# Optimization experiments

Hardware: AMD Instinct MI355X
Metric: run time of the kernel (lower is better)

Reference implementation:

```python
import jax, jax.numpy as jnp
import numpy as np

N_GROUPS = 20000
K = 12
C_IN = 256
C_CH = 128
EPS = 1e-5


def _layernorm(x, g, b):
    mu = jnp.mean(x, axis=-1, keepdims=True)
    var = jnp.mean((x - mu) ** 2, axis=-1, keepdims=True)
    return (x - mu) * jax.lax.rsqrt(var + EPS) * g + b


def _linear(x, W, b):
    # torch nn.Linear: y = x @ W.T + b, W: [out, in]
    return x @ W.T + b


def setup_inputs() -> dict:
    key = jax.random.key(0)
    ks = jax.random.split(key, 16)
    nnz = N_GROUPS * K
    s_in = 1.0 / np.sqrt(C_IN)
    s_ch = 1.0 / np.sqrt(C_CH)
    return {
        "values": jax.random.normal(ks[0], (nnz, C_IN), jnp.float32),
        "ln_in_g": jnp.ones((C_IN,), jnp.float32),
        "ln_in_b": jnp.zeros((C_IN,), jnp.float32),
        "W_ga": jax.random.normal(ks[1], (C_CH, C_IN), jnp.float32) * s_in,
        "b_ga": jax.random.normal(ks[2], (C_CH,), jnp.float32) * 0.02,
        "W_la": jax.random.normal(ks[3], (C_CH, C_IN), jnp.float32) * s_in,
        "b_la": jnp.zeros((C_CH,), jnp.float32),
        "W_gb": jax.random.normal(ks[4], (C_CH, C_IN), jnp.float32) * s_in,
        "b_gb": jax.random.normal(ks[5], (C_CH,), jnp.float32) * 0.02,
        "W_lb": jax.random.normal(ks[6], (C_CH, C_IN), jnp.float32) * s_in,
        "b_lb": jnp.zeros((C_CH,), jnp.float32),
        "ln_o_g": jnp.ones((C_CH,), jnp.float32),
        "ln_o_b": jnp.zeros((C_CH,), jnp.float32),
        "W_go": jax.random.normal(ks[7], (C_IN, C_IN), jnp.float32) * s_in,
        "b_go": jax.random.normal(ks[8], (C_IN,), jnp.float32) * 0.02,
        "W_lo": jax.random.normal(ks[9], (C_IN, C_CH), jnp.float32) * s_ch,
        "b_lo": jax.random.normal(ks[10], (C_IN,), jnp.float32) * 0.02,
        "indices": jax.random.randint(ks[11], (4, nnz), 0, 20000, jnp.int64 if jax.config.jax_enable_x64 else jnp.int32),
    }


def reference(values, ln_in_g, ln_in_b, W_ga, b_ga, W_la, b_la, W_gb, b_gb,
              W_lb, b_lb, ln_o_g, ln_o_b, W_go, b_go, W_lo, b_lo, indices):
    nnz = values.shape[0]
    # input layer norm over channel dim of sparse values
    x = _layernorm(values, ln_in_g, ln_in_b)  # [nnz, C_IN]
    # gated projections to channel_dim
    a = jax.nn.sigmoid(_linear(x, W_ga, b_ga)) * _linear(x, W_la, b_la)  # [nnz, C_CH]
    b = jax.nn.sigmoid(_linear(x, W_gb, b_gb)) * _linear(x, W_lb, b_lb)
    a = a.reshape(nnz // K, K, C_CH)
    b = b.reshape(nnz // K, K, C_CH)
    # axis == 1: einsum('iko,jko->iko', a, b) = a * sum_j b[j]
    tri = a * jnp.sum(b, axis=0, keepdims=True)  # [nnz//K, K, C_CH]
    tri = tri.reshape(nnz, C_CH)
    # output: gate on x times linear of normed triangular update
    out = jax.nn.sigmoid(_linear(x, W_go, b_go)) * _linear(
        _layernorm(tri, ln_o_g, ln_o_b), W_lo, b_lo)  # [nnz, C_IN]
    return out
```

## Files before the change

kernel.cpp:

```cpp
#include <hip/hip_runtime.h>


#define NNZ   240000
#define ROWS  64
#define NBLK  (NNZ / ROWS)
#define PSLOTS 32

typedef __attribute__((ext_vector_type(8))) short bf16x8;
typedef __attribute__((ext_vector_type(4))) float f32x4;
typedef __attribute__((ext_vector_type(8))) _Float16 f16x8;

__device__ __forceinline__ unsigned short f2bf(float f) {
  unsigned int u = __float_as_uint(f);
  u += 0x7fffu + ((u >> 16) & 1u);
  return (unsigned short)(u >> 16);
}
__device__ __forceinline__ float bf2f(unsigned short h) {
  return __uint_as_float(((unsigned int)h) << 16);
}

__global__ __launch_bounds__(256) void prep_kernel(
    const float* __restrict__ Wga, const float* __restrict__ Wla,
    const float* __restrict__ Wgb, const float* __restrict__ Wlb,
    const float* __restrict__ Wgo, const float* __restrict__ Wlo,
    unsigned short* __restrict__ wcat, unsigned short* __restrict__ wgo16,
    unsigned short* __restrict__ wlo16, float* __restrict__ bsum,
    float* __restrict__ bpart)
{
  const int tid = blockIdx.x * 256 + threadIdx.x;
  if (tid < 12 * 128) bsum[tid] = 0.f;
  if (tid < PSLOTS * 1536) bpart[tid] = 0.f;
  if (tid < 131072) {
    const int w8 = tid & 7, c = tid >> 3;
    const int m = c & 15, q = (c >> 4) & 3, t = (c >> 6) & 3;
    const int kb = (c >> 8) & 7, wv = c >> 11;
    const int k = kb * 32 + q * 8 + w8;
    const int ch = ((wv & 3) << 5) + ((t & 1) << 4) + m;
    const float* src = (wv < 4) ? (t < 2 ? Wga : Wla) : (t < 2 ? Wgb : Wlb);
    wcat[tid] = f2bf(src[ch * 256 + k]);
  } else if (tid < 196608) {
    const int o = tid - 131072;
    const int w8 = o & 7, c = o >> 3;
    const int m = c & 15, q = (c >> 4) & 3, nt = (c >> 6) & 1;
    const int kb = (c >> 7) & 7, wv = c >> 10;
    wgo16[o] = f2bf(Wgo[(wv * 32 + nt * 16 + m) * 256 + kb * 32 + q * 8 + w8]);
  } else if (tid < 229376) {
    const int o = tid - 196608;
    const int w8 = o & 7, c = o >> 3;
    const int m = c & 15, q = (c >> 4) & 3, nt = (c >> 6) & 1;
    const int kb = (c >> 7) & 3, wv = c >> 9;
    wlo16[o] = f2bf(Wlo[(wv * 32 + nt * 16 + m) * 128 + kb * 32 + q * 8 + w8]);
  }
}

__global__ __launch_bounds__(512, 4) void k1_kernel(
    const float* __restrict__ values,
    const float* __restrict__ ln_g, const float* __restrict__ ln_b,
    const float* __restrict__ b_ga, const float* __restrict__ b_la,
    const float* __restrict__ b_gb, const float* __restrict__ b_lb,
    const float* __restrict__ b_go,
    const unsigned short* __restrict__ wcat,
    const unsigned short* __restrict__ wgo,
    _Float16* __restrict__ g_ws,
    unsigned short* __restrict__ a_ws,
    float* __restrict__ bpart)
{
  __shared__ unsigned short x_lds[ROWS][256];
  __shared__ float b_raw[ROWS][132];
  const int tid = threadIdx.x;
  const int rbase = blockIdx.x * ROWS;

  {
    const int r = tid >> 3, j = tid & 7;
    const size_t grow = (size_t)(rbase + r) * 256;
    float4 v[8];
    float s1 = 0.f, s2 = 0.f;
#pragma unroll
    for (int i = 0; i < 4; i++) {
      const int e = (j + 8 * i) * 8;
      const float4 t0 = *(const float4*)(values + grow + e);
      const float4 t1 = *(const float4*)(values + grow + e + 4);
      v[2 * i] = t0; v[2 * i + 1] = t1;
      s1 += t0.x + t0.y + t0.z + t0.w + t1.x + t1.y + t1.z + t1.w;
      s2 += t0.x * t0.x + t0.y * t0.y + t0.z * t0.z + t0.w * t0.w
          + t1.x * t1.x + t1.y * t1.y + t1.z * t1.z + t1.w * t1.w;
    }
    s1 += __shfl_xor(s1, 1); s1 += __shfl_xor(s1, 2); s1 += __shfl_xor(s1, 4);
    s2 += __shfl_xor(s2, 1); s2 += __shfl_xor(s2, 2); s2 += __shfl_xor(s2, 4);
    const float mu = s1 * (1.f / 256.f);
    const float rstd = rsqrtf(s2 * (1.f / 256.f) - mu * mu + 1e-5f);
    const int jp = j ^ (r & 7);
#pragma unroll
    for (int i = 0; i < 4; i++) {
      const int e = (j + 8 * i) * 8;
      const float4 a0 = v[2 * i], a1 = v[2 * i + 1];
      const float4 g0 = *(const float4*)(ln_g + e);
      const float4 g1 = *(const float4*)(ln_g + e + 4);
      const float4 c0 = *(const float4*)(ln_b + e);
      const float4 c1 = *(const float4*)(ln_b + e + 4);
      bf16x8 h;
      h[0] = (short)f2bf((a0.x - mu) * rstd * g0.x + c0.x);
      h[1] = (short)f2bf((a0.y - mu) * rstd * g0.y + c0.y);
      h[2] = (short)f2bf((a0.z - mu) * rstd * g0.z + c0.z);
      h[3] = (short)f2bf((a0.w - mu) * rstd * g0.w + c0.w);
      h[4] = (short)f2bf((a1.x - mu) * rstd * g1.x + c1.x);
      h[5] = (short)f2bf((a1.y - mu) * rstd * g1.y + c1.y);
      h[6] = (short)f2bf((a1.z - mu) * rstd * g1.z + c1.z);
      h[7] = (short)f2bf((a1.w - mu) * rstd * g1.w + c1.w);
      *(bf16x8*)&x_lds[r][(jp + 8 * i) * 8] = h;
    }
  }
  __syncthreads();

  const int wv = tid >> 6;
  const int lane = tid & 63;
  const int m = lane & 15, q = lane >> 4;

  {
    f32x4 acc[4][4];
#pragma unroll
    for (int a = 0; a < 4; a++)
#pragma unroll
      for (int b = 0; b < 4; b++) acc[a][b] = (f32x4){0.f, 0.f, 0.f, 0.f};

#pragma unroll
    for (int kb = 0; kb < 8; kb++) {
      bf16x8 A[4], B[4];
#pragma unroll
      for (int mt = 0; mt < 4; mt++)
        A[mt] = *(const bf16x8*)&x_lds[mt * 16 + m][((kb * 4 + q) ^ (m & 7)) << 3];
#pragma unroll
      for (int t = 0; t < 4; t++)
        B[t] = *(const bf16x8*)(wcat + ((((wv * 8 + kb) * 4 + t) * 64 + lane) << 3));
#pragma unroll
      for (int t = 0; t < 4; t++)
#pragma unroll
        for (int mt = 0; mt < 4; mt++)
          acc[mt][t] = __builtin_amdgcn_mfma_f32_16x16x32_bf16(A[mt], B[t], acc[mt][t], 0, 0, 0);
    }

    const bool isA = (wv < 4);
    const int chbase = (wv & 3) * 32;
    const float* bgp = isA ? b_ga : b_gb;
    const float* blp = isA ? b_la : b_lb;
#pragma unroll
    for (int t = 0; t < 2; t++) {
      const int ch = chbase + t * 16 + m;
      const float bgv = bgp[ch], blv = blp[ch];
#pragma unroll
      for (int mt = 0; mt < 4; mt++) {
#pragma unroll
        for (int rg = 0; rg < 4; rg++) {
          const int lrow = mt * 16 + q * 4 + rg;
          const float gv = acc[mt][t][rg] + bgv;
          const float lv = acc[mt][t + 2][rg] + blv;
          const float val = lv / (1.f + __expf(-gv));
          if (isA) {
            a_ws[(size_t)(rbase + lrow) * 128 + ch] = f2bf(val);
          } else {
            b_raw[lrow][ch] = val;
          }
        }
      }
    }
  }

  {
    f32x4 g2[4][2];
#pragma unroll
    for (int a = 0; a < 4; a++)
#pragma unroll
      for (int b = 0; b < 2; b++) g2[a][b] = (f32x4){0.f, 0.f, 0.f, 0.f};

#pragma unroll
    for (int kb = 0; kb < 8; kb++) {
      bf16x8 A[4], B[2];
#pragma unroll
      for (int mt = 0; mt < 4; mt++)
        A[mt] = *(const bf16x8*)&x_lds[mt * 16 + m][((kb * 4 + q) ^ (m & 7)) << 3];
#pragma unroll
      for (int nt = 0; nt < 2; nt++)
        B[nt] = *(const bf16x8*)(wgo + ((((wv * 8 + kb) * 2 + nt) * 64 + lane) << 3));
#pragma unroll
      for (int nt = 0; nt < 2; nt++)
#pragma unroll
        for (int mt = 0; mt < 4; mt++)
          g2[mt][nt] = __builtin_amdgcn_mfma_f32_16x16x32_bf16(A[mt], B[nt], g2[mt][nt], 0, 0, 0);
    }

    const int n0 = wv * 32;
    f16x8 hv[4];
#pragma unroll
    for (int nt = 0; nt < 2; nt++) {
      const float bg = b_go[n0 + nt * 16 + m];
#pragma unroll
      for (int mt = 0; mt < 4; mt++) {
#pragma unroll
        for (int rg = 0; rg < 4; rg++) {
          const float gv = g2[mt][nt][rg] + bg;
          const float s = 1.f / (1.f + __expf(-gv));
          const int idx = (mt * 4 + rg) * 2 + nt;
          hv[idx >> 3][idx & 7] = (_Float16)s;
        }
      }
    }
    _Float16* gd = g_ws + ((((size_t)blockIdx.x) * 8 + wv) * 64 + lane) * 32;
#pragma unroll
    for (int i = 0; i < 4; i++)
      *(f16x8*)(gd + i * 8) = hv[i];
  }
  __syncthreads();

  const int rb12 = rbase % 12;
  float* dst = bpart + (blockIdx.x & (PSLOTS - 1)) * 1536;
#pragma unroll
  for (int it = 0; it < 3; it++) {
    const int s = tid + it * 512;
    const int k12 = s >> 7, ch = s & 127;
    int r0 = k12 - rb12; if (r0 < 0) r0 += 12;
    float sum = 0.f;
    for (int r = r0; r < ROWS; r += 12) sum += b_raw[r][ch];
    atomicAdd(&dst[s], sum);
  }
}

__global__ __launch_bounds__(256) void reduce_kernel(
    const float* __restrict__ bpart, float* __restrict__ bsum)
{
  const int c = blockIdx.x * 256 + threadIdx.x;
  float s = 0.f;
#pragma unroll
  for (int sl = 0; sl < PSLOTS; sl++) s += bpart[sl * 1536 + c];
  bsum[c] = s;
}

__global__ __launch_bounds__(512, 6) void k2_kernel(
    const _Float16* __restrict__ g_ws,
    const unsigned short* __restrict__ a_ws,
    const float* __restrict__ bsum,
    const float* __restrict__ ln_g, const float* __restrict__ ln_b,
    const unsigned short* __restrict__ wlo,
    const float* __restrict__ b_lo,
    float* __restrict__ out)
{
  __shared__ unsigned short t_lds[ROWS][128];
  const int tid = threadIdx.x;
  const int rbase = blockIdx.x * ROWS;

  {
    const int r = tid >> 3, j = tid & 7;
    const int row = rbase + r;
    const int k12 = row % 12;
    const unsigned short* ar = a_ws + (size_t)row * 128;
    const float* bs = bsum + k12 * 128;
    float tv[16];
    float s1 = 0.f, s2 = 0.f;
#pragma unroll
    for (int i = 0; i < 2; i++) {
      const int e = (j + 8 * i) * 8;
      const ushort4 a0 = *(const ushort4*)(ar + e);
      const ushort4 a1 = *(const ushort4*)(ar + e + 4);
      const float4 b0 = *(const float4*)(bs + e);
      const float4 b1 = *(const float4*)(bs + e + 4);
      const float t0 = bf2f(a0.x) * b0.x, t1 = bf2f(a0.y) * b0.y;
      const float t2 = bf2f(a0.z) * b0.z, t3 = bf2f(a0.w) * b0.w;
      const float t4 = bf2f(a1.x) * b1.x, t5 = bf2f(a1.y) * b1.y;
      const float t6 = bf2f(a1.z) * b1.z, t7 = bf2f(a1.w) * b1.w;
      tv[8*i+0] = t0; tv[8*i+1] = t1; tv[8*i+2] = t2; tv[8*i+3] = t3;
      tv[8*i+4] = t4; tv[8*i+5] = t5; tv[8*i+6] = t6; tv[8*i+7] = t7;
      s1 += t0 + t1 + t2 + t3 + t4 + t5 + t6 + t7;
      s2 += t0*t0 + t1*t1 + t2*t2 + t3*t3 + t4*t4 + t5*t5 + t6*t6 + t7*t7;
    }
    s1 += __shfl_xor(s1, 1); s1 += __shfl_xor(s1, 2); s1 += __shfl_xor(s1, 4);
    s2 += __shfl_xor(s2, 1); s2 += __shfl_xor(s2, 2); s2 += __shfl_xor(s2, 4);
    const float mu = s1 * (1.f / 128.f);
    const float rstd = rsqrtf(s2 * (1.f / 128.f) - mu * mu + 1e-5f);
    const int jp = j ^ (r & 7);
#pragma unroll
    for (int i = 0; i < 2; i++) {
      const int e = (j + 8 * i) * 8;
      const float4 g0 = *(const float4*)(ln_g + e);
      const float4 g1 = *(const float4*)(ln_g + e + 4);
      const float4 c0 = *(const float4*)(ln_b + e);
      const float4 c1 = *(const float4*)(ln_b + e + 4);
      bf16x8 h;
      h[0] = (short)f2bf((tv[8*i+0] - mu) * rstd * g0.x + c0.x);
      h[1] = (short)f2bf((tv[8*i+1] - mu) * rstd * g0.y + c0.y);
      h[2] = (short)f2bf((tv[8*i+2] - mu) * rstd * g0.z + c0.z);
      h[3] = (short)f2bf((tv[8*i+3] - mu) * rstd * g0.w + c0.w);
      h[4] = (short)f2bf((tv[8*i+4] - mu) * rstd * g1.x + c1.x);
      h[5] = (short)f2bf((tv[8*i+5] - mu) * rstd * g1.y + c1.y);
      h[6] = (short)f2bf((tv[8*i+6] - mu) * rstd * g1.z + c1.z);
      h[7] = (short)f2bf((tv[8*i+7] - mu) * rstd * g1.w + c1.w);
      *(bf16x8*)&t_lds[r][(jp + 8 * i) * 8] = h;
    }
  }
  __syncthreads();

  const int wv = tid >> 6, lane = tid & 63;
  const int m = lane & 15, q = lane >> 4;

  const _Float16* gs = g_ws + ((((size_t)blockIdx.x) * 8 + wv) * 64 + lane) * 32;
  f16x8 gh[4];
#pragma unroll
  for (int i = 0; i < 4; i++)
    gh[i] = *(const f16x8*)(gs + i * 8);

  f32x4 al[4][2];
#pragma unroll
  for (int a = 0; a < 4; a++)
#pragma unroll
    for (int b = 0; b < 2; b++) al[a][b] = (f32x4){0.f, 0.f, 0.f, 0.f};

#pragma unroll
  for (int kb = 0; kb < 4; kb++) {
    bf16x8 A[4], B[2];
#pragma unroll
    for (int mt = 0; mt < 4; mt++)
      A[mt] = *(const bf16x8*)&t_lds[mt * 16 + m][((kb * 4 + q) ^ (m & 7)) << 3];
#pragma unroll
    for (int nt = 0; nt < 2; nt++)
      B[nt] = *(const bf16x8*)(wlo + ((((wv * 4 + kb) * 2 + nt) * 64 + lane) << 3));
#pragma unroll
    for (int nt = 0; nt < 2; nt++)
#pragma unroll
      for (int mt = 0; mt < 4; mt++)
        al[mt][nt] = __builtin_amdgcn_mfma_f32_16x16x32_bf16(A[mt], B[nt], al[mt][nt], 0, 0, 0);
  }

#pragma unroll
  for (int nt = 0; nt < 2; nt++) {
    const int n = wv * 32 + nt * 16 + m;
    const float blo = b_lo[n];
#pragma unroll
    for (int mt = 0; mt < 4; mt++) {
#pragma unroll
      for (int rg = 0; rg < 4; rg++) {
        const int row = rbase + mt * 16 + q * 4 + rg;
        const int idx = (mt * 4 + rg) * 2 + nt;
        const float gval = (float)gh[idx >> 3][idx & 7];
        out[(size_t)row * 256 + n] = gval * (al[mt][nt][rg] + blo);
      }
    }
  }
}

extern "C" void kernel_launch(void* const* d_in, const int* in_sizes, int n_in,
                              void* d_out, int out_size, void* d_ws, size_t ws_size,
                              hipStream_t stream) {
  (void)in_sizes; (void)n_in; (void)out_size; (void)ws_size;
  const float* values  = (const float*)d_in[0];
  const float* ln_in_g = (const float*)d_in[1];
  const float* ln_in_b = (const float*)d_in[2];
  const float* W_ga = (const float*)d_in[3];
  const float* b_ga = (const float*)d_in[4];
  const float* W_la = (const float*)d_in[5];
  const float* b_la = (const float*)d_in[6];
  const float* W_gb = (const float*)d_in[7];
  const float* b_gb = (const float*)d_in[8];
  const float* W_lb = (const float*)d_in[9];
  const float* b_lb = (const float*)d_in[10];
  const float* ln_o_g = (const float*)d_in[11];
  const float* ln_o_b = (const float*)d_in[12];
  const float* W_go = (const float*)d_in[13];
  const float* b_go = (const float*)d_in[14];
  const float* W_lo = (const float*)d_in[15];
  const float* b_lo = (const float*)d_in[16];

  char* ws = (char*)d_ws;
  _Float16*       g_ws  = (_Float16*)      (ws + 0);
  unsigned short* a_ws  = (unsigned short*)(ws + 122880000);
  unsigned short* wcat  = (unsigned short*)(ws + 184320000);
  unsigned short* wgo16 = (unsigned short*)(ws + 184582144);
  unsigned short* wlo16 = (unsigned short*)(ws + 184713216);
  float*          bsum  = (float*)        (ws + 184778752);
  float*          bpart = (float*)        (ws + 184784896);

  hipLaunchKernelGGL(prep_kernel, dim3(896), dim3(256), 0, stream,
                     W_ga, W_la, W_gb, W_lb, W_go, W_lo, wcat, wgo16, wlo16,
                     bsum, bpart);
  hipLaunchKernelGGL(k1_kernel, dim3(NBLK), dim3(512), 0, stream,
                     values, ln_in_g, ln_in_b, b_ga, b_la, b_gb, b_lb, b_go,
                     wcat, wgo16, g_ws, a_ws, bpart);
  hipLaunchKernelGGL(reduce_kernel, dim3(6), dim3(256), 0, stream,
                     bpart, bsum);
  hipLaunchKernelGGL(k2_kernel, dim3(NBLK), dim3(512), 0, stream,
                     g_ws, a_ws, bsum, ln_o_g, ln_o_b, wlo16, b_lo,
                     (float*)d_out);
}
```

Measured before the change: 662.3 us.

## Store x in MFMA fragment layout and drop LDS staging in k2

In k1, x is now written to LDS in MFMA-fragment order, so each lane's A operand becomes one contiguous 16-byte read with no XOR swizzle. The gate workspace changes to a lane-interleaved layout for coalesced stores. k2 is restructured into a 2x4 wave tiling that loads a_ws fragments directly from global memory, computes the layernorm with cross-quad shuffles, and feeds the MFMAs from registers, removing its LDS buffer and a __syncthreads. The cost is higher register pressure, so k2's occupancy hint drops from 6 to 4 blocks, and the fragment-order LDS writes may cause bank conflicts.

```diff
diff --git a/kernel.cpp b/kernel.cpp
--- a/kernel.cpp
+++ b/kernel.cpp
@@ -65,7 +65,7 @@
     unsigned short* __restrict__ a_ws,
     float* __restrict__ bpart)
 {
-  __shared__ unsigned short x_lds[ROWS][256];
+  __shared__ unsigned short x_lds[16384];
   __shared__ float b_raw[ROWS][132];
   const int tid = threadIdx.x;
   const int rbase = blockIdx.x * ROWS;
@@ -89,10 +89,11 @@
     s2 += __shfl_xor(s2, 1); s2 += __shfl_xor(s2, 2); s2 += __shfl_xor(s2, 4);
     const float mu = s1 * (1.f / 256.f);
     const float rstd = rsqrtf(s2 * (1.f / 256.f) - mu * mu + 1e-5f);
-    const int jp = j ^ (r & 7);
+    const int m = r & 15, mt = r >> 4;
 #pragma unroll
     for (int i = 0; i < 4; i++) {
-      const int e = (j + 8 * i) * 8;
+      const int c8 = j + 8 * i;
+      const int e = c8 * 8;
       const float4 a0 = v[2 * i], a1 = v[2 * i + 1];
       const float4 g0 = *(const float4*)(ln_g + e);
       const float4 g1 = *(const float4*)(ln_g + e + 4);
@@ -107,7 +108,8 @@
       h[5] = (short)f2bf((a1.y - mu) * rstd * g1.y + c1.y);
       h[6] = (short)f2bf((a1.z - mu) * rstd * g1.z + c1.z);
       h[7] = (short)f2bf((a1.w - mu) * rstd * g1.w + c1.w);
-      *(bf16x8*)&x_lds[r][(jp + 8 * i) * 8] = h;
+      const int off = (((c8 >> 2) * 4 + mt) * 64 + (c8 & 3) * 16 + m) * 8;
+      *(bf16x8*)&x_lds[off] = h;
     }
   }
   __syncthreads();
@@ -128,7 +130,7 @@
       bf16x8 A[4], B[4];
 #pragma unroll
       for (int mt = 0; mt < 4; mt++)
-        A[mt] = *(const bf16x8*)&x_lds[mt * 16 + m][((kb * 4 + q) ^ (m & 7)) << 3];
+        A[mt] = *(const bf16x8*)&x_lds[((kb * 4 + mt) * 64 + lane) * 8];
 #pragma unroll
       for (int t = 0; t < 4; t++)
         B[t] = *(const bf16x8*)(wcat + ((((wv * 8 + kb) * 4 + t) * 64 + lane) << 3));
@@ -177,7 +179,7 @@
       bf16x8 A[4], B[2];
 #pragma unroll
       for (int mt = 0; mt < 4; mt++)
-        A[mt] = *(const bf16x8*)&x_lds[mt * 16 + m][((kb * 4 + q) ^ (m & 7)) << 3];
+        A[mt] = *(const bf16x8*)&x_lds[((kb * 4 + mt) * 64 + lane) * 8];
 #pragma unroll
       for (int nt = 0; nt < 2; nt++)
         B[nt] = *(const bf16x8*)(wgo + ((((wv * 8 + kb) * 2 + nt) * 64 + lane) << 3));
@@ -204,10 +206,10 @@
         }
       }
     }
-    _Float16* gd = g_ws + ((((size_t)blockIdx.x) * 8 + wv) * 64 + lane) * 32;
+    _Float16* gd = g_ws + ((size_t)blockIdx.x * 8 + wv) * 2048;
 #pragma unroll
     for (int i = 0; i < 4; i++)
-      *(f16x8*)(gd + i * 8) = hv[i];
+      *(f16x8*)(gd + i * 512 + lane * 8) = hv[i];
   }
   __syncthreads();
 
@@ -234,7 +236,7 @@
   bsum[c] = s;
 }
 
-__global__ __launch_bounds__(512, 6) void k2_kernel(
+__global__ __launch_bounds__(512, 4) void k2_kernel(
     const _Float16* __restrict__ g_ws,
     const unsigned short* __restrict__ a_ws,
     const float* __restrict__ bsum,
@@ -243,102 +245,110 @@
     const float* __restrict__ b_lo,
     float* __restrict__ out)
 {
-  __shared__ unsigned short t_lds[ROWS][128];
   const int tid = threadIdx.x;
   const int rbase = blockIdx.x * ROWS;
-
-  {
-    const int r = tid >> 3, j = tid & 7;
-    const int row = rbase + r;
-    const int k12 = row % 12;
-    const unsigned short* ar = a_ws + (size_t)row * 128;
-    const float* bs = bsum + k12 * 128;
-    float tv[16];
+  const int wv = tid >> 6, lane = tid & 63;
+  const int m = lane & 15, q = lane >> 4;
+  const int wr = wv >> 2, wc = wv & 3;
+
+  f16x8 gh[2][2];
+#pragma unroll
+  for (int s = 0; s < 2; s++)
+#pragma unroll
+    for (int c = 0; c < 2; c++)
+      gh[s][c] = *(const f16x8*)(g_ws +
+          (((size_t)blockIdx.x * 8 + wc * 2 + s) * 4 + wr * 2 + c) * 512 + lane * 8);
+
+  bf16x8 afr[2][4];
+#pragma unroll
+  for (int mt = 0; mt < 2; mt++) {
+    const unsigned short* ap =
+        a_ws + (size_t)(rbase + wr * 32 + mt * 16 + m) * 128 + q * 8;
+#pragma unroll
+    for (int kb = 0; kb < 4; kb++)
+      afr[mt][kb] = *(const bf16x8*)(ap + kb * 32);
+  }
+
+  bf16x8 tfr[2][4];
+#pragma unroll
+  for (int mt = 0; mt < 2; mt++) {
+    const int row = rbase + wr * 32 + mt * 16 + m;
+    const float* bs = bsum + (row % 12) * 128 + q * 8;
+    float tv[32];
     float s1 = 0.f, s2 = 0.f;
 #pragma unroll
-    for (int i = 0; i < 2; i++) {
-      const int e = (j + 8 * i) * 8;
-      const ushort4 a0 = *(const ushort4*)(ar + e);
-      const ushort4 a1 = *(const ushort4*)(ar + e + 4);
-      const float4 b0 = *(const float4*)(bs + e);
-      const float4 b1 = *(const float4*)(bs + e + 4);
-      const float t0 = bf2f(a0.x) * b0.x, t1 = bf2f(a0.y) * b0.y;
-      const float t2 = bf2f(a0.z) * b0.z, t3 = bf2f(a0.w) * b0.w;
-      const float t4 = bf2f(a1.x) * b1.x, t5 = bf2f(a1.y) * b1.y;
-      const float t6 = bf2f(a1.z) * b1.z, t7 = bf2f(a1.w) * b1.w;
-      tv[8*i+0] = t0; tv[8*i+1] = t1; tv[8*i+2] = t2; tv[8*i+3] = t3;
-      tv[8*i+4] = t4; tv[8*i+5] = t5; tv[8*i+6] = t6; tv[8*i+7] = t7;
+    for (int kb = 0; kb < 4; kb++) {
+      const float4 b0 = *(const float4*)(bs + kb * 32);
+      const float4 b1 = *(const float4*)(bs + kb * 32 + 4);
+      const bf16x8 a8 = afr[mt][kb];
+      const float t0 = bf2f((unsigned short)a8[0]) * b0.x;
+      const float t1 = bf2f((unsigned short)a8[1]) * b0.y;
+      const float t2 = bf2f((unsigned short)a8[2]) * b0.z;
+      const float t3 = bf2f((unsigned short)a8[3]) * b0.w;
+      const float t4 = bf2f((unsigned short)a8[4]) * b1.x;
+      const float t5 = bf2f((unsigned short)a8[5]) * b1.y;
+      const float t6 = bf2f((unsigned short)a8[6]) * b1.z;
+      const float t7 = bf2f((unsigned short)a8[7]) * b1.w;
+      tv[kb*8+0] = t0; tv[kb*8+1] = t1; tv[kb*8+2] = t2; tv[kb*8+3] = t3;
+      tv[kb*8+4] = t4; tv[kb*8+5] = t5; tv[kb*8+6] = t6; tv[kb*8+7] = t7;
       s1 += t0 + t1 + t2 + t3 + t4 + t5 + t6 + t7;
       s2 += t0*t0 + t1*t1 + t2*t2 + t3*t3 + t4*t4 + t5*t5 + t6*t6 + t7*t7;
     }
-    s1 += __shfl_xor(s1, 1); s1 += __shfl_xor(s1, 2); s1 += __shfl_xor(s1, 4);
-    s2 += __shfl_xor(s2, 1); s2 += __shfl_xor(s2, 2); s2 += __shfl_xor(s2, 4);
+    s1 += __shfl_xor(s1, 16); s1 += __shfl_xor(s1, 32);
+    s2 += __shfl_xor(s2, 16); s2 += __shfl_xor(s2, 32);
     const float mu = s1 * (1.f / 128.f);
     const float rstd = rsqrtf(s2 * (1.f / 128.f) - mu * mu + 1e-5f);
-    const int jp = j ^ (r & 7);
-#pragma unroll
-    for (int i = 0; i < 2; i++) {
-      const int e = (j + 8 * i) * 8;
+#pragma unroll
+    for (int kb = 0; kb < 4; kb++) {
+      const int e = kb * 32 + q * 8;
       const float4 g0 = *(const float4*)(ln_g + e);
       const float4 g1 = *(const float4*)(ln_g + e + 4);
       const float4 c0 = *(const float4*)(ln_b + e);
       const float4 c1 = *(const float4*)(ln_b + e + 4);
       bf16x8 h;
-      h[0] = (short)f2bf((tv[8*i+0] - mu) * rstd * g0.x + c0.x);
-      h[1] = (short)f2bf((tv[8*i+1] - mu) * rstd * g0.y + c0.y);
-      h[2] = (short)f2bf((tv[8*i+2] - mu) * rstd * g0.z + c0.z);
-      h[3] = (short)f2bf((tv[8*i+3] - mu) * rstd * g0.w + c0.w);
-      h[4] = (short)f2bf((tv[8*i+4] - mu) * rstd * g1.x + c1.x);
-      h[5] = (short)f2bf((tv[8*i+5] - mu) * rstd * g1.y + c1.y);
-      h[6] = (short)f2bf((tv[8*i+6] - mu) * rstd * g1.z + c1.z);
-      h[7] = (short)f2bf((tv[8*i+7] - mu) * rstd * g1.w + c1.w);
-      *(bf16x8*)&t_lds[r][(jp + 8 * i) * 8] = h;
-    }
-  }
-  __syncthreads();
-
-  const int wv = tid >> 6, lane = tid & 63;
-  const int m = lane & 15, q = lane >> 4;
-
-  const _Float16* gs = g_ws + ((((size_t)blockIdx.x) * 8 + wv) * 64 + lane) * 32;
-  f16x8 gh[4];
-#pragma unroll
-  for (int i = 0; i < 4; i++)
-    gh[i] = *(const f16x8*)(gs + i * 8);
-
-  f32x4 al[4][2];
-#pragma unroll
-  for (int a = 0; a < 4; a++)
-#pragma unroll
-    for (int b = 0; b < 2; b++) al[a][b] = (f32x4){0.f, 0.f, 0.f, 0.f};
+      h[0] = (short)f2bf((tv[kb*8+0] - mu) * rstd * g0.x + c0.x);
+      h[1] = (short)f2bf((tv[kb*8+1] - mu) * rstd * g0.y + c0.y);
+      h[2] = (short)f2bf((tv[kb*8+2] - mu) * rstd * g0.z + c0.z);
+      h[3] = (short)f2bf((tv[kb*8+3] - mu) * rstd * g0.w + c0.w);
+      h[4] = (short)f2bf((tv[kb*8+4] - mu) * rstd * g1.x + c1.x);
+      h[5] = (short)f2bf((tv[kb*8+5] - mu) * rstd * g1.y + c1.y);
+      h[6] = (short)f2bf((tv[kb*8+6] - mu) * rstd * g1.z + c1.z);
+      h[7] = (short)f2bf((tv[kb*8+7] - mu) * rstd * g1.w + c1.w);
+      tfr[mt][kb] = h;
+    }
+  }
+
+  f32x4 al[2][4];
+#pragma unroll
+  for (int a = 0; a < 2; a++)
+#pragma unroll
+    for (int b = 0; b < 4; b++) al[a][b] = (f32x4){0.f, 0.f, 0.f, 0.f};
 
 #pragma unroll
   for (int kb = 0; kb < 4; kb++) {
-    bf16x8 A[4], B[2];
-#pragma unroll
-    for (int mt = 0; mt < 4; mt++)
-      A[mt] = *(const bf16x8*)&t_lds[mt * 16 + m][((kb * 4 + q) ^ (m & 7)) << 3];
-#pragma unroll
-    for (int nt = 0; nt < 2; nt++)
-      B[nt] = *(const bf16x8*)(wlo + ((((wv * 4 + kb) * 2 + nt) * 64 + lane) << 3));
-#pragma unroll
-    for (int nt = 0; nt < 2; nt++)
-#pragma unroll
-      for (int mt = 0; mt < 4; mt++)
-        al[mt][nt] = __builtin_amdgcn_mfma_f32_16x16x32_bf16(A[mt], B[nt], al[mt][nt], 0, 0, 0);
-  }
-
-#pragma unroll
-  for (int nt = 0; nt < 2; nt++) {
-    const int n = wv * 32 + nt * 16 + m;
+    bf16x8 B[4];
+#pragma unroll
+    for (int nt = 0; nt < 4; nt++)
+      B[nt] = *(const bf16x8*)(wlo +
+          (((((wc * 2 + (nt >> 1)) * 4 + kb) * 2 + (nt & 1)) * 64 + lane) << 3));
+#pragma unroll
+    for (int nt = 0; nt < 4; nt++)
+#pragma unroll
+      for (int mt = 0; mt < 2; mt++)
+        al[mt][nt] = __builtin_amdgcn_mfma_f32_16x16x32_bf16(tfr[mt][kb], B[nt], al[mt][nt], 0, 0, 0);
+  }
+
+#pragma unroll
+  for (int nt = 0; nt < 4; nt++) {
+    const int n = wc * 64 + nt * 16 + m;
     const float blo = b_lo[n];
 #pragma unroll
-    for (int mt = 0; mt < 4; mt++) {
+    for (int mt = 0; mt < 2; mt++) {
 #pragma unroll
       for (int rg = 0; rg < 4; rg++) {
-        const int row = rbase + mt * 16 + q * 4 + rg;
-        const int idx = (mt * 4 + rg) * 2 + nt;
-        const float gval = (float)gh[idx >> 3][idx & 7];
+        const int row = rbase + wr * 32 + mt * 16 + q * 4 + rg;
+        const int il = ((mt * 4 + rg) * 2 + (nt & 1));
+        const float gval = (float)gh[nt >> 1][il >> 3][il & 7];
         out[(size_t)row * 256 + n] = gval * (al[mt][nt][rg] + blo);
       }
     }
```

Result: slower. 1.049 ms (+58.4%).

## Alias k1 LDS buffers, reorder gate GEMM first, coalesce g_ws layout

Applied to the files above, without the earlier changes.

In k1 the output-gate GEMM now runs before the main gated-projection GEMM, which lets x_lds and b_raw share one LDS allocation: the x tile is dead by the time b_raw is written, with a barrier placed between them. The launch-bounds minimum-blocks hint rises from 4 to 8 to raise occupancy. The g_ws gate layout becomes lane-interleaved so its stores and loads coalesce across the wavefront, and k2 loads the a row as one 16-byte vector instead of two 8-byte ones. The higher occupancy target may force register spills, since the 4x4 accumulator tile stays live.

```diff
diff --git a/kernel.cpp b/kernel.cpp
--- a/kernel.cpp
+++ b/kernel.cpp
@@ -53,7 +53,7 @@
   }
 }
 
-__global__ __launch_bounds__(512, 4) void k1_kernel(
+__global__ __launch_bounds__(512, 8) void k1_kernel(
     const float* __restrict__ values,
     const float* __restrict__ ln_g, const float* __restrict__ ln_b,
     const float* __restrict__ b_ga, const float* __restrict__ b_la,
@@ -65,8 +65,9 @@
     unsigned short* __restrict__ a_ws,
     float* __restrict__ bpart)
 {
-  __shared__ unsigned short x_lds[ROWS][256];
-  __shared__ float b_raw[ROWS][132];
+  __shared__ float smem[ROWS * 132];
+  float (*b_raw)[132] = (float(*)[132])smem;
+  unsigned short (*x_lds)[256] = (unsigned short(*)[256])smem;
   const int tid = threadIdx.x;
   const int rbase = blockIdx.x * ROWS;
 
@@ -107,7 +108,8 @@
       h[5] = (short)f2bf((a1.y - mu) * rstd * g1.y + c1.y);
       h[6] = (short)f2bf((a1.z - mu) * rstd * g1.z + c1.z);
       h[7] = (short)f2bf((a1.w - mu) * rstd * g1.w + c1.w);
-      *(bf16x8*)&x_lds[r][(jp + 8 * i) * 8] = h;
+      const int p = (jp + 8 * i) * 8;
+      *(bf16x8*)&x_lds[r][p] = h;
     }
   }
   __syncthreads();
@@ -117,28 +119,75 @@
   const int m = lane & 15, q = lane >> 4;
 
   {
-    f32x4 acc[4][4];
+    f32x4 g2[4][2];
 #pragma unroll
     for (int a = 0; a < 4; a++)
 #pragma unroll
-      for (int b = 0; b < 4; b++) acc[a][b] = (f32x4){0.f, 0.f, 0.f, 0.f};
+      for (int b = 0; b < 2; b++) g2[a][b] = (f32x4){0.f, 0.f, 0.f, 0.f};
 
 #pragma unroll
     for (int kb = 0; kb < 8; kb++) {
-      bf16x8 A[4], B[4];
+      bf16x8 A[4], B[2];
 #pragma unroll
       for (int mt = 0; mt < 4; mt++)
         A[mt] = *(const bf16x8*)&x_lds[mt * 16 + m][((kb * 4 + q) ^ (m & 7)) << 3];
 #pragma unroll
-      for (int t = 0; t < 4; t++)
-        B[t] = *(const bf16x8*)(wcat + ((((wv * 8 + kb) * 4 + t) * 64 + lane) << 3));
-#pragma unroll
-      for (int t = 0; t < 4; t++)
+      for (int nt = 0; nt < 2; nt++)
+        B[nt] = *(const bf16x8*)(wgo + ((((wv * 8 + kb) * 2 + nt) * 64 + lane) << 3));
+#pragma unroll
+      for (int nt = 0; nt < 2; nt++)
 #pragma unroll
         for (int mt = 0; mt < 4; mt++)
-          acc[mt][t] = __builtin_amdgcn_mfma_f32_16x16x32_bf16(A[mt], B[t], acc[mt][t], 0, 0, 0);
-    }
-
+          g2[mt][nt] = __builtin_amdgcn_mfma_f32_16x16x32_bf16(A[mt], B[nt], g2[mt][nt], 0, 0, 0);
+    }
+
+    const int n0 = wv * 32;
+    f16x8 hv[4];
+#pragma unroll
+    for (int nt = 0; nt < 2; nt++) {
+      const float bg = b_go[n0 + nt * 16 + m];
+#pragma unroll
+      for (int mt = 0; mt < 4; mt++) {
+#pragma unroll
+        for (int rg = 0; rg < 4; rg++) {
+          const float gv = g2[mt][nt][rg] + bg;
+          const float s = 1.f / (1.f + __expf(-gv));
+          const int idx = (mt * 4 + rg) * 2 + nt;
+          hv[idx >> 3][idx & 7] = (_Float16)s;
+        }
+      }
+    }
+    _Float16* gd = g_ws + ((size_t)blockIdx.x * 8 + wv) * 2048;
+#pragma unroll
+    for (int i = 0; i < 4; i++)
+      *(f16x8*)(gd + i * 512 + lane * 8) = hv[i];
+  }
+
+  f32x4 acc[4][4];
+#pragma unroll
+  for (int a = 0; a < 4; a++)
+#pragma unroll
+    for (int b = 0; b < 4; b++) acc[a][b] = (f32x4){0.f, 0.f, 0.f, 0.f};
+
+#pragma unroll
+  for (int kb = 0; kb < 8; kb++) {
+    bf16x8 A[4], B[4];
+#pragma unroll
+    for (int mt = 0; mt < 4; mt++)
+      A[mt] = *(const bf16x8*)&x_lds[mt * 16 + m][((kb * 4 + q) ^ (m & 7)) << 3];
+#pragma unroll
+    for (int t = 0; t < 4; t++)
+      B[t] = *(const bf16x8*)(wcat + ((((wv * 8 + kb) * 4 + t) * 64 + lane) << 3));
+#pragma unroll
+    for (int t = 0; t < 4; t++)
+#pragma unroll
+      for (int mt = 0; mt < 4; mt++)
+        acc[mt][t] = __builtin_amdgcn_mfma_f32_16x16x32_bf16(A[mt], B[t], acc[mt][t], 0, 0, 0);
+  }
+
+  __syncthreads();
+
+  {
     const bool isA = (wv < 4);
     const int chbase = (wv & 3) * 32;
     const float* bgp = isA ? b_ga : b_gb;
@@ -164,51 +213,6 @@
       }
     }
   }
-
-  {
-    f32x4 g2[4][2];
-#pragma unroll
-    for (int a = 0; a < 4; a++)
-#pragma unroll
-      for (int b = 0; b < 2; b++) g2[a][b] = (f32x4){0.f, 0.f, 0.f, 0.f};
-
-#pragma unroll
-    for (int kb = 0; kb < 8; kb++) {
-      bf16x8 A[4], B[2];
-#pragma unroll
-      for (int mt = 0; mt < 4; mt++)
-        A[mt] = *(const bf16x8*)&x_lds[mt * 16 + m][((kb * 4 + q) ^ (m & 7)) << 3];
-#pragma unroll
-      for (int nt = 0; nt < 2; nt++)
-        B[nt] = *(const bf16x8*)(wgo + ((((wv * 8 + kb) * 2 + nt) * 64 + lane) << 3));
-#pragma unroll
-      for (int nt = 0; nt < 2; nt++)
-#pragma unroll
-        for (int mt = 0; mt < 4; mt++)
-          g2[mt][nt] = __builtin_amdgcn_mfma_f32_16x16x32_bf16(A[mt], B[nt], g2[mt][nt], 0, 0, 0);
-    }
-
-    const int n0 = wv * 32;
-    f16x8 hv[4];
-#pragma unroll
-    for (int nt = 0; nt < 2; nt++) {
-      const float bg = b_go[n0 + nt * 16 + m];
-#pragma unroll
-      for (int mt = 0; mt < 4; mt++) {
-#pragma unroll
-        for (int rg = 0; rg < 4; rg++) {
-          const float gv = g2[mt][nt][rg] + bg;
-          const float s = 1.f / (1.f + __expf(-gv));
-          const int idx = (mt * 4 + rg) * 2 + nt;
-          hv[idx >> 3][idx & 7] = (_Float16)s;
-        }
-      }
-    }
-    _Float16* gd = g_ws + ((((size_t)blockIdx.x) * 8 + wv) * 64 + lane) * 32;
-#pragma unroll
-    for (int i = 0; i < 4; i++)
-      *(f16x8*)(gd + i * 8) = hv[i];
-  }
   __syncthreads();
 
   const int rb12 = rbase % 12;
@@ -258,14 +262,17 @@
 #pragma unroll
     for (int i = 0; i < 2; i++) {
       const int e = (j + 8 * i) * 8;
-      const ushort4 a0 = *(const ushort4*)(ar + e);
-      const ushort4 a1 = *(const ushort4*)(ar + e + 4);
+      const bf16x8 a8 = *(const bf16x8*)(ar + e);
       const float4 b0 = *(const float4*)(bs + e);
       const float4 b1 = *(const float4*)(bs + e + 4);
-      const float t0 = bf2f(a0.x) * b0.x, t1 = bf2f(a0.y) * b0.y;
-      const float t2 = bf2f(a0.z) * b0.z, t3 = bf2f(a0.w) * b0.w;
-      const float t4 = bf2f(a1.x) * b1.x, t5 = bf2f(a1.y) * b1.y;
-      const float t6 = bf2f(a1.z) * b1.z, t7 = bf2f(a1.w) * b1.w;
+      const float t0 = bf2f((unsigned short)a8[0]) * b0.x;
+      const float t1 = bf2f((unsigned short)a8[1]) * b0.y;
+      const float t2 = bf2f((unsigned short)a8[2]) * b0.z;
+      const float t3 = bf2f((unsigned short)a8[3]) * b0.w;
+      const float t4 = bf2f((unsigned short)a8[4]) * b1.x;
+      const float t5 = bf2f((unsigned short)a8[5]) * b1.y;
+      const float t6 = bf2f((unsigned short)a8[6]) * b1.z;
+      const float t7 = bf2f((unsigned short)a8[7]) * b1.w;
       tv[8*i+0] = t0; tv[8*i+1] = t1; tv[8*i+2] = t2; tv[8*i+3] = t3;
       tv[8*i+4] = t4; tv[8*i+5] = t5; tv[8*i+6] = t6; tv[8*i+7] = t7;
       s1 += t0 + t1 + t2 + t3 + t4 + t5 + t6 + t7;
@@ -300,11 +307,11 @@
   const int wv = tid >> 6, lane = tid & 63;
   const int m = lane & 15, q = lane >> 4;
 
-  const _Float16* gs = g_ws + ((((size_t)blockIdx.x) * 8 + wv) * 64 + lane) * 32;
+  const _Float16* gs = g_ws + ((size_t)blockIdx.x * 8 + wv) * 2048 + lane * 8;
   f16x8 gh[4];
 #pragma unroll
   for (int i = 0; i < 4; i++)
-    gh[i] = *(const f16x8*)(gs + i * 8);
+    gh[i] = *(const f16x8*)(gs + i * 512);
 
   f32x4 al[4][2];
 #pragma unroll
```

Result: slower. 1.744 ms (+163.3%).
